# Kernel tuning notes

Measured on AMD Instinct MI355X. Metric: run time of the kernel, lower is better.

The kernel has to match this reference:

```python
import jax, jax.numpy as jnp
import numpy as np

# --- instant-NGP style multiresolution hash encoding config ---
L = 16          # levels
T = 524288      # hash table size (2**19)
D = 3           # input (spatial) dim
F = 2           # features per level
N_PTS = 500000  # query points
RES_MIN, RES_MAX = 16.0, 512.0

# spatial-hash primes from the source (first D entries; 1 for dim 0)
PRIMES = jnp.array([1, 2654435761, 805459861, 3674653429, 2097192037, 1434869437, 2165219737][:D], dtype=jnp.uint32)

# geometric resolution schedule N_l = floor(RES_MIN * b**l)
_b = np.exp((np.log(RES_MAX) - np.log(RES_MIN)) / (L - 1))
RES = jnp.asarray(np.floor(RES_MIN * _b ** np.arange(L)), dtype=jnp.float32)  # [L]

# the 2**D hypercube corner offsets, corner c has bit d = (c>>d)&1
OFFSETS = jnp.array([[(c >> d) & 1 for d in range(D)] for c in range(2 ** D)], dtype=jnp.uint32)  # [8, D]


def setup_inputs() -> dict:
    k1, k2 = jax.random.split(jax.random.key(0))
    x = jax.random.uniform(k1, (N_PTS, D), dtype=jnp.float32)          # coords in [0,1)
    hash_tables = jax.random.normal(k2, (L, T, F), dtype=jnp.float32) * 1e-4
    return {"x": x, "hash_tables": hash_tables}


def reference(x, hash_tables):
    N = x.shape[0]
    scaled = x[:, None, :] * RES[None, :, None]          # [N, L, D]
    floor = jnp.floor(scaled)
    w = scaled - floor                                    # [N, L, D] interpolation weights
    floor_u = floor.astype(jnp.uint32)

    # spatial hash of the 2**D corners: XOR-reduce(coord_d * prime_d) mod T.
    # loop over the D (=3) coordinate dims to avoid a [N,L,8,D] corner tensor.
    h = jnp.zeros((N, L, 2 ** D), dtype=jnp.uint32)
    for d in range(D):
        corner_d = floor_u[:, :, None, d] + OFFSETS[None, None, :, d]  # [N, L, 8], uint32 wrap
        h = h ^ (corner_d * PRIMES[d])
    idx = (h % jnp.uint32(T)).astype(jnp.int32)           # [N, L, 8]

    # gather per-level features: hash_tables[l, idx[n,l,c]] -> [N, L, 8, F]
    feats = hash_tables[jnp.arange(L)[None, :, None], idx]

    # D-linear interpolation weights: prod_d (w_d if corner bit set else 1-w_d)
    wd = jnp.where(OFFSETS[None, None, :, :] == 1, w[:, :, None, :], 1.0 - w[:, :, None, :])  # [N,L,8,D]
    weights = wd.prod(axis=-1)                            # [N, L, 8]

    out = (feats * weights[..., None]).sum(axis=2)        # [N, L, F]
    return out.reshape(N, L * F)
```

## Files before the change

kernel.cpp:

```cpp
#include <hip/hip_runtime.h>
#include <math.h>

#define NPTS 500000
#define TSIZE 524288u
#define TMASK (TSIZE - 1u)
#define CHUNKS 1954
#define SLICE 245

struct ResArgs { float r[16]; };

__device__ __forceinline__ float2 mhe_point_level(
    const float* __restrict__ x, const float* __restrict__ tbl,
    int p, int l, float res)
{
    float x0 = x[p * 3 + 0];
    float x1 = x[p * 3 + 1];
    float x2 = x[p * 3 + 2];

    float s0 = x0 * res, s1 = x1 * res, s2 = x2 * res;
    float f0 = floorf(s0), f1 = floorf(s1), f2 = floorf(s2);
    float w0 = s0 - f0, w1 = s1 - f1, w2 = s2 - f2;
    unsigned u0 = (unsigned)f0, u1 = (unsigned)f1, u2 = (unsigned)f2;

    unsigned b0 = u1 * 2654435761u, b1 = (u1 + 1u) * 2654435761u;
    unsigned c0 = u2 * 805459861u,  c1 = (u2 + 1u) * 805459861u;

    const float2* t  = (const float2*)tbl + (size_t)l * TSIZE;
    const float4* t4 = (const float4*)t;

    float v0a = 1.f - w0, v0b = w0;
    float v1a = 1.f - w1, v1b = w1;
    float v2a = 1.f - w2, v2b = w2;

    bool odd = (u0 & 1u) != 0u;
    unsigned u0p1 = u0 + 1u;

    float o0 = 0.f, o1 = 0.f;
#pragma unroll
    for (int j = 0; j < 4; ++j) {
        unsigned bc = ((j & 1) ? b1 : b0) ^ ((j & 2) ? c1 : c0);
        unsigned e0 = (u0 ^ bc) & TMASK;
        float4 q = t4[e0 >> 1];
        float2 lo = make_float2(q.x, q.y);
        float2 hi = make_float2(q.z, q.w);
        float2 fc0 = (e0 & 1u) ? hi : lo;
        float2 fc1 = (e0 & 1u) ? lo : hi;
        if (odd) {
            unsigned e1 = (u0p1 ^ bc) & TMASK;
            fc1 = t[e1];
        }
        float wyz = ((j & 1) ? v1b : v1a) * ((j & 2) ? v2b : v2a);
        o0 = fmaf(v0a * wyz, fc0.x, o0);
        o1 = fmaf(v0a * wyz, fc0.y, o1);
        o0 = fmaf(v0b * wyz, fc1.x, o0);
        o1 = fmaf(v0b * wyz, fc1.y, o1);
    }
    return make_float2(o0, o1);
}

__global__ __launch_bounds__(256) void mhe_gather(
    const float* __restrict__ x,
    const float* __restrict__ tbl,
    float2* __restrict__ ws,
    ResArgs ra)
{
    int b = blockIdx.x;
    int xcd = b & 7;
    int t = b >> 3;
    int l, chunk;
    if (t < CHUNKS) {
        l = 8 + xcd;
        chunk = t;
    } else {
        int u = t - CHUNKS;
        int pl = u / SLICE;
        int sc = u - pl * SLICE;
        l = pl;
        chunk = xcd * SLICE + sc;
        if (chunk >= CHUNKS) return;
    }
    int p = chunk * 256 + threadIdx.x;
    if (p >= NPTS) return;

    float2 o = mhe_point_level(x, tbl, p, l, ra.r[l]);
    ws[(size_t)l * NPTS + p] = o;
}

__global__ __launch_bounds__(256) void mhe_transpose(
    const float2* __restrict__ ws, float2* __restrict__ out)
{
    __shared__ float2 tile[16][65];
    int p0 = blockIdx.x * 64;
    int t = threadIdx.x;

    int pc = t & 63;
#pragma unroll
    for (int i = 0; i < 4; ++i) {
        int l = (t >> 6) + i * 4;
        int p = p0 + pc;
        if (p < NPTS) tile[l][pc] = ws[(size_t)l * NPTS + p];
    }
    __syncthreads();

#pragma unroll
    for (int i = 0; i < 4; ++i) {
        int pp = (t >> 4) + i * 16;
        int l = t & 15;
        int p = p0 + pp;
        if (p < NPTS) out[(size_t)p * 16 + l] = tile[l][pp];
    }
}

__global__ __launch_bounds__(256) void mhe_kernel(
    const float* __restrict__ x,
    const float* __restrict__ tbl,
    float* __restrict__ out,
    ResArgs ra)
{
    int gid = blockIdx.x * 256 + threadIdx.x;
    int p = gid >> 4;
    int l = gid & 15;
    if (p >= NPTS) return;
    float2 o = mhe_point_level(x, tbl, p, l, ra.r[l]);
    ((float2*)out)[(size_t)p * 16 + l] = o;
}

extern "C" void kernel_launch(void* const* d_in, const int* in_sizes, int n_in,
                              void* d_out, int out_size, void* d_ws, size_t ws_size,
                              hipStream_t stream) {
    const float* x   = (const float*)d_in[0];
    const float* tbl = (const float*)d_in[1];
    float* out = (float*)d_out;

    ResArgs ra;
    double bb = exp((log(512.0) - log(16.0)) / 15.0);
    for (int l = 0; l < 16; ++l)
        ra.r[l] = (float)floor(16.0 * pow(bb, (double)l));

    size_t ws_needed = (size_t)NPTS * 16 * sizeof(float2);
    if (ws_size >= ws_needed) {
        int tasks_per_xcd = CHUNKS + 8 * SLICE;
        mhe_gather<<<8 * tasks_per_xcd, 256, 0, stream>>>(x, tbl, (float2*)d_ws, ra);
        mhe_transpose<<<(NPTS + 63) / 64, 256, 0, stream>>>((const float2*)d_ws,
                                                            (float2*)out);
    } else {
        mhe_kernel<<<(NPTS * 16 + 255) / 256, 256, 0, stream>>>(x, tbl, out, ra);
    }
}
```

Baseline: 221.2 us.

## Stage coarse-level hash table blocks in LDS for levels 0 and 1

Result: no change. 222.5 us (+0.6%).

```diff
diff --git a/kernel.cpp b/kernel.cpp
--- a/kernel.cpp
+++ b/kernel.cpp
@@ -6,6 +6,7 @@
 #define TMASK (TSIZE - 1u)
 #define CHUNKS 1954
 #define SLICE 245
+#define POOL_LVLS 6
 
 struct ResArgs { float r[16]; };
 
@@ -75,7 +76,7 @@
         int u = t - CHUNKS;
         int pl = u / SLICE;
         int sc = u - pl * SLICE;
-        l = pl;
+        l = 2 + pl;
         chunk = xcd * SLICE + sc;
         if (chunk >= CHUNKS) return;
     }
@@ -84,6 +85,61 @@
 
     float2 o = mhe_point_level(x, tbl, p, l, ra.r[l]);
     ws[(size_t)l * NPTS + p] = o;
+}
+
+template <int LVL, int RESI>
+__global__ __launch_bounds__(1024) void mhe_staged(
+    const float* __restrict__ x,
+    const float* __restrict__ tbl,
+    float2* __restrict__ ws,
+    float res)
+{
+    extern __shared__ float2 st[];
+    const float2* t = (const float2*)tbl + (size_t)LVL * TSIZE;
+    int tid = threadIdx.x;
+
+    for (int b = tid >> 5; b < RESI * RESI; b += 32) {
+        unsigned u1 = (unsigned)(b / RESI), u2 = (unsigned)(b % RESI);
+        unsigned base = ((u1 * 2654435761u) ^ (u2 * 805459861u)) & TMASK & ~31u;
+        st[b * 32 + (tid & 31)] = t[base + (tid & 31)];
+    }
+    __syncthreads();
+
+    int p = blockIdx.x * 1024 + tid;
+    if (p >= NPTS) return;
+
+    float x0 = x[p * 3 + 0];
+    float x1 = x[p * 3 + 1];
+    float x2 = x[p * 3 + 2];
+    float s0 = x0 * res, s1 = x1 * res, s2 = x2 * res;
+    float f0 = floorf(s0), f1 = floorf(s1), f2 = floorf(s2);
+    float w0 = s0 - f0, w1 = s1 - f1, w2 = s2 - f2;
+    unsigned u0 = (unsigned)f0, u1 = (unsigned)f1, u2 = (unsigned)f2;
+
+    unsigned b0 = u1 * 2654435761u, b1 = (u1 + 1u) * 2654435761u;
+    unsigned c0 = u2 * 805459861u,  c1 = (u2 + 1u) * 805459861u;
+
+    float v0a = 1.f - w0, v0b = w0;
+    float v1a = 1.f - w1, v1b = w1;
+    float v2a = 1.f - w2, v2b = w2;
+
+    float o0 = 0.f, o1 = 0.f;
+#pragma unroll
+    for (int j = 0; j < 4; ++j) {
+        unsigned u1c = u1 + ((j & 1) ? 1u : 0u);
+        unsigned u2c = u2 + ((j & 2) ? 1u : 0u);
+        unsigned bc = ((j & 1) ? b1 : b0) ^ ((j & 2) ? c1 : c0);
+        int blk = (int)(u1c * RESI + u2c) * 32;
+        unsigned bc5 = bc & 31u;
+        float2 fc0 = st[blk + (int)(u0 ^ bc5)];
+        float2 fc1 = st[blk + (int)((u0 + 1u) ^ bc5)];
+        float wyz = ((j & 1) ? v1b : v1a) * ((j & 2) ? v2b : v2a);
+        o0 = fmaf(v0a * wyz, fc0.x, o0);
+        o1 = fmaf(v0a * wyz, fc0.y, o1);
+        o0 = fmaf(v0b * wyz, fc1.x, o0);
+        o1 = fmaf(v0b * wyz, fc1.y, o1);
+    }
+    ws[(size_t)LVL * NPTS + p] = make_float2(o0, o1);
 }
 
 __global__ __launch_bounds__(256) void mhe_transpose(
@@ -139,8 +195,22 @@
 
     size_t ws_needed = (size_t)NPTS * 16 * sizeof(float2);
     if (ws_size >= ws_needed) {
-        int tasks_per_xcd = CHUNKS + 8 * SLICE;
+        (void)hipFuncSetAttribute((const void*)mhe_staged<0, 17>,
+                                  hipFuncAttributeMaxDynamicSharedMemorySize,
+                                  17 * 17 * 32 * (int)sizeof(float2));
+        (void)hipFuncSetAttribute((const void*)mhe_staged<1, 21>,
+                                  hipFuncAttributeMaxDynamicSharedMemorySize,
+                                  21 * 21 * 32 * (int)sizeof(float2));
+
+        int tasks_per_xcd = CHUNKS + POOL_LVLS * SLICE;
         mhe_gather<<<8 * tasks_per_xcd, 256, 0, stream>>>(x, tbl, (float2*)d_ws, ra);
+
+        int sb = (NPTS + 1023) / 1024;
+        mhe_staged<0, 17><<<sb, 1024, 17 * 17 * 32 * sizeof(float2), stream>>>(
+            x, tbl, (float2*)d_ws, ra.r[0]);
+        mhe_staged<1, 21><<<sb, 1024, 21 * 21 * 32 * sizeof(float2), stream>>>(
+            x, tbl, (float2*)d_ws, ra.r[1]);
+
         mhe_transpose<<<(NPTS + 63) / 64, 256, 0, stream>>>((const float2*)d_ws,
                                                             (float2*)out);
     } else {
```

## Sort points by Morton bucket before hash gather to improve table locality

Applied to the files above, without the earlier changes.

Result: slower. 227.2 us (+2.7%).

```diff
diff --git a/kernel.cpp b/kernel.cpp
--- a/kernel.cpp
+++ b/kernel.cpp
@@ -6,17 +6,14 @@
 #define TMASK (TSIZE - 1u)
 #define CHUNKS 1954
 #define SLICE 245
+#define NBKT 32768
 
 struct ResArgs { float r[16]; };
 
-__device__ __forceinline__ float2 mhe_point_level(
-    const float* __restrict__ x, const float* __restrict__ tbl,
-    int p, int l, float res)
-{
-    float x0 = x[p * 3 + 0];
-    float x1 = x[p * 3 + 1];
-    float x2 = x[p * 3 + 2];
-
+__device__ __forceinline__ float2 mhe_core(
+    float x0, float x1, float x2,
+    const float* __restrict__ tbl, int l, float res)
+{
     float s0 = x0 * res, s1 = x1 * res, s2 = x2 * res;
     float f0 = floorf(s0), f1 = floorf(s1), f2 = floorf(s2);
     float w0 = s0 - f0, w1 = s1 - f1, w2 = s2 - f2;
@@ -58,11 +55,66 @@
     return make_float2(o0, o1);
 }
 
+__device__ __forceinline__ unsigned mspread5(unsigned v) {
+    return (v & 1u) | ((v & 2u) << 2) | ((v & 4u) << 4)
+         | ((v & 8u) << 6) | ((v & 16u) << 8);
+}
+__device__ __forceinline__ unsigned bucket_of(float x0, float x1, float x2) {
+    unsigned bx = (unsigned)min(31, (int)(x0 * 32.f));
+    unsigned by = (unsigned)min(31, (int)(x1 * 32.f));
+    unsigned bz = (unsigned)min(31, (int)(x2 * 32.f));
+    return mspread5(bx) | (mspread5(by) << 1) | (mspread5(bz) << 2);
+}
+
+__global__ __launch_bounds__(256) void sort_count(
+    const float* __restrict__ x, int* __restrict__ hist)
+{
+    int p = blockIdx.x * 256 + threadIdx.x;
+    if (p >= NPTS) return;
+    unsigned b = bucket_of(x[p * 3], x[p * 3 + 1], x[p * 3 + 2]);
+    atomicAdd(&hist[b], 1);
+}
+
+__global__ __launch_bounds__(1024) void sort_scan(
+    const int* __restrict__ hist, int* __restrict__ ofs)
+{
+    __shared__ int sums[1024];
+    int t = threadIdx.x;
+    int base = t * 32;
+    int loc[32];
+    int s = 0;
+#pragma unroll
+    for (int i = 0; i < 32; ++i) { loc[i] = hist[base + i]; s += loc[i]; }
+    sums[t] = s;
+    __syncthreads();
+    for (int off = 1; off < 1024; off <<= 1) {
+        int v = (t >= off) ? sums[t - off] : 0;
+        __syncthreads();
+        sums[t] += v;
+        __syncthreads();
+    }
+    int run = sums[t] - s;
+#pragma unroll
+    for (int i = 0; i < 32; ++i) { ofs[base + i] = run; run += loc[i]; }
+}
+
+__global__ __launch_bounds__(256) void sort_scatter(
+    const float* __restrict__ x, int* __restrict__ ofs,
+    float4* __restrict__ sx, int* __restrict__ perm)
+{
+    int p = blockIdx.x * 256 + threadIdx.x;
+    if (p >= NPTS) return;
+    float x0 = x[p * 3], x1 = x[p * 3 + 1], x2 = x[p * 3 + 2];
+    unsigned b = bucket_of(x0, x1, x2);
+    int pos = atomicAdd(&ofs[b], 1);
+    sx[pos] = make_float4(x0, x1, x2, 0.f);
+    perm[pos] = p;
+}
+
+template <bool SORTED>
 __global__ __launch_bounds__(256) void mhe_gather(
-    const float* __restrict__ x,
-    const float* __restrict__ tbl,
-    float2* __restrict__ ws,
-    ResArgs ra)
+    const float* __restrict__ x, const float4* __restrict__ sx,
+    const float* __restrict__ tbl, float2* __restrict__ ws, ResArgs ra)
 {
     int b = blockIdx.x;
     int xcd = b & 7;
@@ -82,14 +134,21 @@
     int p = chunk * 256 + threadIdx.x;
     if (p >= NPTS) return;
 
-    float2 o = mhe_point_level(x, tbl, p, l, ra.r[l]);
+    float x0, x1, x2;
+    if (SORTED) { float4 v = sx[p]; x0 = v.x; x1 = v.y; x2 = v.z; }
+    else        { x0 = x[p * 3]; x1 = x[p * 3 + 1]; x2 = x[p * 3 + 2]; }
+
+    float2 o = mhe_core(x0, x1, x2, tbl, l, ra.r[l]);
     ws[(size_t)l * NPTS + p] = o;
 }
 
+template <bool PERM>
 __global__ __launch_bounds__(256) void mhe_transpose(
-    const float2* __restrict__ ws, float2* __restrict__ out)
+    const float2* __restrict__ ws, const int* __restrict__ perm,
+    float2* __restrict__ out)
 {
     __shared__ float2 tile[16][65];
+    __shared__ int pidx[64];
     int p0 = blockIdx.x * 64;
     int t = threadIdx.x;
 
@@ -100,28 +159,35 @@
         int p = p0 + pc;
         if (p < NPTS) tile[l][pc] = ws[(size_t)l * NPTS + p];
     }
+    if (PERM && t < 64) {
+        int p = p0 + t;
+        pidx[t] = (p < NPTS) ? perm[p] : 0;
+    }
     __syncthreads();
 
-#pragma unroll
-    for (int i = 0; i < 4; ++i) {
-        int pp = (t >> 4) + i * 16;
-        int l = t & 15;
-        int p = p0 + pp;
-        if (p < NPTS) out[(size_t)p * 16 + l] = tile[l][pp];
-    }
-}
-
-__global__ __launch_bounds__(256) void mhe_kernel(
-    const float* __restrict__ x,
-    const float* __restrict__ tbl,
-    float* __restrict__ out,
-    ResArgs ra)
+    float4* out4 = (float4*)out;
+#pragma unroll
+    for (int i = 0; i < 2; ++i) {
+        int idx = t + i * 256;
+        int pt = idx >> 3, q = idx & 7;
+        int p = p0 + pt;
+        if (p >= NPTS) continue;
+        int dp = PERM ? pidx[pt] : p;
+        float2 a = tile[2 * q][pt];
+        float2 b2 = tile[2 * q + 1][pt];
+        out4[(size_t)dp * 8 + q] = make_float4(a.x, a.y, b2.x, b2.y);
+    }
+}
+
+__global__ __launch_bounds__(256) void mhe_direct(
+    const float* __restrict__ x, const float* __restrict__ tbl,
+    float* __restrict__ out, ResArgs ra)
 {
     int gid = blockIdx.x * 256 + threadIdx.x;
     int p = gid >> 4;
     int l = gid & 15;
     if (p >= NPTS) return;
-    float2 o = mhe_point_level(x, tbl, p, l, ra.r[l]);
+    float2 o = mhe_core(x[p * 3], x[p * 3 + 1], x[p * 3 + 2], tbl, l, ra.r[l]);
     ((float2*)out)[(size_t)p * 16 + l] = o;
 }
 
@@ -137,13 +203,40 @@
     for (int l = 0; l < 16; ++l)
         ra.r[l] = (float)floor(16.0 * pow(bb, (double)l));
 
-    size_t ws_needed = (size_t)NPTS * 16 * sizeof(float2);
-    if (ws_size >= ws_needed) {
-        int tasks_per_xcd = CHUNKS + 8 * SLICE;
-        mhe_gather<<<8 * tasks_per_xcd, 256, 0, stream>>>(x, tbl, (float2*)d_ws, ra);
-        mhe_transpose<<<(NPTS + 63) / 64, 256, 0, stream>>>((const float2*)d_ws,
-                                                            (float2*)out);
+    const size_t WS_LV   = 0;
+    const size_t WS_SX   = 64000000;
+    const size_t WS_PERM = 72000000;
+    const size_t WS_HIST = 74000000;
+    const size_t WS_OFS  = 74131072;
+    const size_t WS_NEW  = 74262144;
+    const size_t WS_T2   = (size_t)NPTS * 16 * sizeof(float2);
+
+    int gather_grid = 8 * (CHUNKS + 8 * SLICE);
+    int tp_grid = (NPTS + 63) / 64;
+
+    if (ws_size >= WS_NEW) {
+        char* w = (char*)d_ws;
+        float2* ws_lv = (float2*)(w + WS_LV);
+        float4* sx    = (float4*)(w + WS_SX);
+        int* perm     = (int*)(w + WS_PERM);
+        int* hist     = (int*)(w + WS_HIST);
+        int* ofs      = (int*)(w + WS_OFS);
+
+        hipMemsetAsync(hist, 0, NBKT * sizeof(int), stream);
+        sort_count<<<CHUNKS, 256, 0, stream>>>(x, hist);
+        sort_scan<<<1, 1024, 0, stream>>>(hist, ofs);
+        sort_scatter<<<CHUNKS, 256, 0, stream>>>(x, ofs, sx, perm);
+
+        mhe_gather<true><<<gather_grid, 256, 0, stream>>>(x, sx, tbl, ws_lv, ra);
+        mhe_transpose<true><<<tp_grid, 256, 0, stream>>>(ws_lv, perm,
+                                                         (float2*)out);
+    } else if (ws_size >= WS_T2) {
+        float2* ws_lv = (float2*)d_ws;
+        mhe_gather<false><<<gather_grid, 256, 0, stream>>>(x, nullptr, tbl,
+                                                           ws_lv, ra);
+        mhe_transpose<false><<<tp_grid, 256, 0, stream>>>(ws_lv, nullptr,
+                                                          (float2*)out);
     } else {
-        mhe_kernel<<<(NPTS * 16 + 255) / 256, 256, 0, stream>>>(x, tbl, out, ra);
-    }
-}
+        mhe_direct<<<(NPTS * 16 + 255) / 256, 256, 0, stream>>>(x, tbl, out, ra);
+    }
+}
```
